# Performance work log

Hardware: AMD Instinct MI355X
Metric: run time of the kernel (lower is better)

Reference implementation:

```python
import jax, jax.numpy as jnp
import numpy as np

N_HIT = 30000   # hits per plane
N_EDGE = 90000  # Delaunay planar edges per plane (~3N)
N_SP = 30000    # spacepoints
H = 128         # hidden dim
F_IN = 4        # wire, time, integral, rms
N_CLASS = 5     # semantic classes
N_ITERS = 3     # core message-passing iterations
PLANES = ("u", "v", "y")


def setup_inputs() -> dict:
    key = jax.random.key(0)
    ks = iter(jax.random.split(key, 64))
    inp = {}
    for p in PLANES:
        inp[f"x_{p}"] = jax.random.normal(next(ks), (N_HIT, F_IN), jnp.float32)
        inp[f"edge_{p}"] = jax.random.randint(next(ks), (2, N_EDGE), 0, N_HIT)
        # row 0: hit index in plane, row 1: spacepoint index
        inp[f"nexus_{p}"] = jax.random.randint(next(ks), (2, N_SP), 0, N_HIT)
    def lin(k, i, o):
        return (jax.random.normal(k, (i, o), jnp.float32) / np.sqrt(i)).astype(jnp.float32)
    inp["W_enc"] = lin(next(ks), F_IN, H); inp["b_enc"] = jnp.zeros((H,), jnp.float32)
    inp["W_msg1"] = lin(next(ks), 2 * H, H); inp["b_msg1"] = jnp.zeros((H,), jnp.float32)
    inp["W_msg2"] = lin(next(ks), H, H); inp["b_msg2"] = jnp.zeros((H,), jnp.float32)
    inp["W_upd"] = lin(next(ks), 2 * H, H); inp["b_upd"] = jnp.zeros((H,), jnp.float32)
    inp["W_sp"] = lin(next(ks), H, H); inp["b_sp"] = jnp.zeros((H,), jnp.float32)
    inp["W_nx"] = lin(next(ks), 2 * H, H); inp["b_nx"] = jnp.zeros((H,), jnp.float32)
    inp["W_sem"] = lin(next(ks), H, N_CLASS); inp["b_sem"] = jnp.zeros((N_CLASS,), jnp.float32)
    return inp


def _segment_mean(data, ids, num):
    s = jax.ops.segment_sum(data, ids, num_segments=num)
    c = jax.ops.segment_sum(jnp.ones((ids.shape[0],), data.dtype), ids, num_segments=num)
    return s / jnp.maximum(c, 1.0)[:, None]


def _core(hs, edges, nexus, W_msg1, b_msg1, W_msg2, b_msg2, W_upd, b_upd,
          W_sp, b_sp, W_nx, b_nx):
    # --- planar convolution per plane (gather-transform-scatter) ---
    new_hs = []
    for h, e in zip(hs, edges):
        src, dst = e[0], e[1]
        m = jnp.concatenate([h[dst], h[src]], axis=-1)          # [E, 2H]
        m = jax.nn.relu(m @ W_msg1 + b_msg1) @ W_msg2 + b_msg2  # [E, H]
        agg = _segment_mean(m, dst, h.shape[0])                 # [N, H]
        upd = jax.nn.relu(jnp.concatenate([h, agg], -1) @ W_upd + b_upd)
        new_hs.append(h + upd)
    hs = new_hs
    # --- nexus convolution: planes -> spacepoints -> planes ---
    sp = jnp.zeros((N_SP, hs[0].shape[1]), hs[0].dtype)
    for h, nx in zip(hs, nexus):
        sp = sp + _segment_mean(h[nx[0]], nx[1], N_SP)
    sp = jax.nn.relu(sp @ W_sp + b_sp)                          # [N_SP, H]
    out_hs = []
    for h, nx in zip(hs, nexus):
        back = _segment_mean(sp[nx[1]], nx[0], h.shape[0])      # [N, H]
        upd = jax.nn.relu(jnp.concatenate([h, back], -1) @ W_nx + b_nx)
        out_hs.append(h + upd)
    return out_hs


def reference(x_u, x_v, x_y, edge_u, edge_v, edge_y, nexus_u, nexus_v, nexus_y,
              W_enc, b_enc, W_msg1, b_msg1, W_msg2, b_msg2, W_upd, b_upd,
              W_sp, b_sp, W_nx, b_nx, W_sem, b_sem):
    edges = (edge_u, edge_v, edge_y)
    nexus = (nexus_u, nexus_v, nexus_y)
    # encoder
    hs = [jax.nn.relu(x @ W_enc + b_enc) for x in (x_u, x_v, x_y)]
    # core message-passing iterations (planar + nexus)
    for _ in range(N_ITERS):
        hs = _core(hs, edges, nexus, W_msg1, b_msg1, W_msg2, b_msg2,
                   W_upd, b_upd, W_sp, b_sp, W_nx, b_nx)
    # semantic decoder per plane
    return tuple(h @ W_sem + b_sem for h in hs)
```

## Files before the change

kernel.cpp:

```cpp
#include <hip/hip_runtime.h>
#include <hip/hip_fp16.h>

#define N_HITS 30000
#define N_EDGES 90000
#define N_SPS 30000
#define HD 128
#define NCLS 5

#define PADM 136

typedef __attribute__((ext_vector_type(8))) _Float16 f16x8;
typedef __attribute__((ext_vector_type(4))) float floatx4;

__device__ __forceinline__ float2 h2f2(uint u) {
    union { uint u; __half2 h; } x; x.u = u;
    return __half22float2(x.h);
}
__device__ __forceinline__ uint f2h2(float a, float b) {
    union { uint u; __half2 h; } x;
    x.h = __halves2half2(__float2half(a), __float2half(b));
    return x.u;
}

__global__ void hist_all_kernel(const int* __restrict__ eu, const int* __restrict__ ev,
                                const int* __restrict__ ey, const int* __restrict__ nu,
                                const int* __restrict__ nv, const int* __restrict__ ny,
                                int* __restrict__ cnt) {
    int gid = blockIdx.x * blockDim.x + threadIdx.x;
    if (gid >= 450000) return;
    int p = gid / 150000;
    int r = gid - p * 150000;
    const int* e = (p == 0) ? eu : (p == 1) ? ev : ey;
    const int* nx = (p == 0) ? nu : (p == 1) ? nv : ny;
    if (r < N_EDGES) {
        atomicAdd(&cnt[p * 30000 + e[N_EDGES + r]], 1);
    } else if (r < N_EDGES + N_SPS) {
        int i = r - N_EDGES;
        atomicAdd(&cnt[(3 + p) * 30000 + nx[N_SPS + i]], 1);
    } else {
        int i = r - N_EDGES - N_SPS;
        atomicAdd(&cnt[(6 + p) * 30000 + nx[i]], 1);
    }
}

__launch_bounds__(1024)
__global__ void scan_kernel(const int* __restrict__ cnt, int* __restrict__ off,
                            int* __restrict__ cursor) {
    int seg = blockIdx.x;
    const int* c = cnt + seg * 30000;
    int* o = off + seg * 30001;
    int* cur = cursor + seg * 30000;
    int t = threadIdx.x;
    int base = t * 30;
    int lc[30];
    int sum = 0;
#pragma unroll
    for (int k = 0; k < 30; ++k) {
        int i = base + k;
        lc[k] = (i < 30000) ? c[i] : 0;
        sum += lc[k];
    }
    __shared__ int part[1024];
    part[t] = sum;
    __syncthreads();
    for (int d = 1; d < 1024; d <<= 1) {
        int x = (t >= d) ? part[t - d] : 0;
        __syncthreads();
        part[t] += x;
        __syncthreads();
    }
    int run = part[t] - sum;
#pragma unroll
    for (int k = 0; k < 30; ++k) {
        int i = base + k;
        if (i < 30000) { o[i] = run; cur[i] = run; run += lc[k]; }
    }
    if (t == 1023) o[30000] = part[1023];
}

__global__ void fill_kernel(const int* __restrict__ eu, const int* __restrict__ ev,
                            const int* __restrict__ ey, const int* __restrict__ nu,
                            const int* __restrict__ nv, const int* __restrict__ ny,
                            int* __restrict__ cursor, int* __restrict__ csr_e,
                            int* __restrict__ csr_s, int* __restrict__ csr_h) {
    int gid = blockIdx.x * blockDim.x + threadIdx.x;
    if (gid >= 450000) return;
    int p = gid / 150000;
    int r = gid - p * 150000;
    const int* e = (p == 0) ? eu : (p == 1) ? ev : ey;
    const int* nx = (p == 0) ? nu : (p == 1) ? nv : ny;
    if (r < N_EDGES) {
        int d = e[N_EDGES + r];
        int pos = atomicAdd(&cursor[p * 30000 + d], 1);
        csr_e[p * N_EDGES + pos] = e[r];
    } else if (r < N_EDGES + N_SPS) {
        int i = r - N_EDGES;
        int spid = nx[N_SPS + i];
        int pos = atomicAdd(&cursor[(3 + p) * 30000 + spid], 1);
        csr_s[p * N_SPS + pos] = nx[i];
    } else {
        int i = r - N_EDGES - N_SPS;
        int hit = nx[i];
        int pos = atomicAdd(&cursor[(6 + p) * 30000 + hit], 1);
        csr_h[p * N_SPS + pos] = nx[N_SPS + i];
    }
}

__device__ __forceinline__ void pack4(const float* __restrict__ W, _Float16* __restrict__ P,
                                      int idx, int koff) {
    int j = idx & 7, lane = (idx >> 3) & 63, ks = (idx >> 9) & 3, n = (idx >> 11) & 7;
    int k = ks * 32 + (lane >> 4) * 8 + j, col = n * 16 + (lane & 15);
    P[idx] = (_Float16)W[(k + koff) * 128 + col];
}
__device__ __forceinline__ void pack8(const float* __restrict__ W, _Float16* __restrict__ P, int idx) {
    int j = idx & 7, lane = (idx >> 3) & 63, ks = (idx >> 9) & 7, n = (idx >> 12) & 7;
    int k = ks * 32 + (lane >> 4) * 8 + j, col = n * 16 + (lane & 15);
    P[idx] = (_Float16)W[k * 128 + col];
}

__global__ void wprep_kernel(const float* __restrict__ W1, const float* __restrict__ W2,
                             const float* __restrict__ Wu, const float* __restrict__ Wn,
                             const float* __restrict__ Wsp, _Float16* __restrict__ packs) {
    int gid = blockIdx.x * blockDim.x + threadIdx.x;
    if (gid < 16384) { pack4(W1, packs, gid, 0); return; }
    gid -= 16384;
    if (gid < 16384) { pack4(W1, packs + 16384, gid, 128); return; }
    gid -= 16384;
    if (gid < 16384) { pack4(W2, packs + 32768, gid, 0); return; }
    gid -= 16384;
    if (gid < 32768) { pack8(Wu, packs + 49152, gid); return; }
    gid -= 32768;
    if (gid < 32768) { pack8(Wn, packs + 81920, gid); return; }
    gid -= 32768;
    if (gid < 16384) { pack4(Wsp, packs + 114688, gid, 0); }
}

__launch_bounds__(256, 4)
__global__ void enc_y_kernel(const float* __restrict__ xu, const float* __restrict__ xv,
                             const float* __restrict__ xy, const float* __restrict__ We,
                             const float* __restrict__ be, const _Float16* __restrict__ W1dP,
                             const _Float16* __restrict__ W1sP, _Float16* __restrict__ h,
                             _Float16* __restrict__ y_d, _Float16* __restrict__ y_s) {
    __shared__ _Float16 sA[128 * PADM];
    __shared__ _Float16 sO[128 * PADM];
    int t = threadIdx.x;
    int n0b = blockIdx.x * 128;
    const int M = 3 * N_HITS;
    for (int i = t; i < 2048; i += 256) {
        int row = i >> 4, c = i & 15;
        int n = n0b + row; if (n >= M) n = M - 1;
        int p = n / N_HITS;
        int nn = n - p * N_HITS;
        const float* x = (p == 0) ? xu : (p == 1) ? xv : xy;
        float4 xv4 = *(const float4*)(x + nn * 4);
        union { _Float16 o8[8]; uint4 u; } outv;
#pragma unroll
        for (int j = 0; j < 8; ++j) {
            int col = c * 8 + j;
            float acc = be[col];
            acc = fmaf(xv4.x, We[0 * HD + col], acc);
            acc = fmaf(xv4.y, We[1 * HD + col], acc);
            acc = fmaf(xv4.z, We[2 * HD + col], acc);
            acc = fmaf(xv4.w, We[3 * HD + col], acc);
            outv.o8[j] = (_Float16)fmaxf(acc, 0.f);
        }
        *(uint4*)&sA[row * PADM + c * 8] = outv.u;
        if (n0b + row < M) ((uint4*)(h + (size_t)n * HD))[c] = outv.u;
    }
    __syncthreads();

    int lane = t & 63, wave = t >> 6;
    int lcol = lane & 15, quad = lane >> 4;
    int nt0 = wave * 2;
    bool odd = (lcol & 1) != 0;

    for (int half = 0; half < 2; ++half) {
        const f16x8* wp = (const f16x8*)(half == 0 ? W1dP : W1sP);
        _Float16* out = half == 0 ? y_d : y_s;
        f16x8 B[2][4];
#pragma unroll
        for (int nt = 0; nt < 2; ++nt)
#pragma unroll
            for (int ks = 0; ks < 4; ++ks)
                B[nt][ks] = wp[((nt0 + nt) * 4 + ks) * 64 + lane];
        floatx4 acc[8][2];
#pragma unroll
        for (int mt = 0; mt < 8; ++mt) { acc[mt][0] = (floatx4){0,0,0,0}; acc[mt][1] = (floatx4){0,0,0,0}; }
#pragma unroll
        for (int mt = 0; mt < 8; ++mt)
#pragma unroll
            for (int ks = 0; ks < 4; ++ks) {
                f16x8 a = *(const f16x8*)&sA[(mt * 16 + lcol) * PADM + ks * 32 + quad * 8];
                acc[mt][0] = __builtin_amdgcn_mfma_f32_16x16x32_f16(a, B[0][ks], acc[mt][0], 0, 0, 0);
                acc[mt][1] = __builtin_amdgcn_mfma_f32_16x16x32_f16(a, B[1][ks], acc[mt][1], 0, 0, 0);
            }
#pragma unroll
        for (int mt = 0; mt < 8; ++mt)
#pragma unroll
            for (int r = 0; r < 4; ++r) {
                float v0 = acc[mt][0][r], v1 = acc[mt][1][r];
                float p0 = __shfl_xor(v0, 1), p1 = __shfl_xor(v1, 1);
                float av = odd ? p1 : v0, bv = odd ? v1 : p0;
                int col = nt0 * 16 + (odd ? 15 + lcol : lcol);
                *(uint*)&sO[(mt * 16 + quad * 4 + r) * PADM + col] = f2h2(av, bv);
            }
        __syncthreads();
        for (int i = t; i < 2048; i += 256) {
            int row = i >> 4, c = i & 15;
            int n = n0b + row;
            if (n < M) ((uint4*)(out + (size_t)n * HD))[c] = *(uint4*)&sO[row * PADM + c * 8];
        }
        __syncthreads();
    }
}

#define ECAP 640
__launch_bounds__(256, 5)
__global__ void update_planar_kernel(_Float16* __restrict__ h, const _Float16* __restrict__ y_d,
                                     const _Float16* __restrict__ y_s,
                                     const int* __restrict__ off, const int* __restrict__ csr_e,
                                     const float* __restrict__ b1,
                                     const _Float16* __restrict__ W2P, const float* __restrict__ b2,
                                     const _Float16* __restrict__ WuP, const float* __restrict__ bu) {
    int p = blockIdx.y;
    _Float16* hp = h + (size_t)p * N_HITS * HD;
    const _Float16* ydp = y_d + (size_t)p * N_HITS * HD;
    const _Float16* ysp = y_s + (size_t)p * N_HITS * HD;
    const int* o = off + p * 30001;
    const int* csr = csr_e + p * N_EDGES;

    __shared__ _Float16 sA[64 * PADM];
    __shared__ int sOff[65];
    __shared__ int sIdx[ECAP];
    int t = threadIdx.x;
    int n0b = blockIdx.x * 64;
    int lane = t & 63, wave = t >> 6;
    int lcol = lane & 15, quad = lane >> 4;
    int nt0 = wave * 2;
    bool odd = (lcol & 1) != 0;

    if (t < 65) {
        int idx = n0b + t; if (idx > N_HITS) idx = N_HITS;
        sOff[t] = o[idx];
    }
    for (int i = t; i < 1024; i += 256) {
        int row = i >> 4, c = i & 15;
        int n = n0b + row; if (n >= N_HITS) n = N_HITS - 1;
        f16x8 yv = *(const f16x8*)&ydp[(size_t)n * HD + c * 8];
        float4 b1a = *(const float4*)(b1 + c * 8);
        float4 b1b = *(const float4*)(b1 + c * 8 + 4);
        float bb[8] = {b1a.x, b1a.y, b1a.z, b1a.w, b1b.x, b1b.y, b1b.z, b1b.w};
        f16x8 ov;
#pragma unroll
        for (int j = 0; j < 8; ++j) ov[j] = (_Float16)((float)yv[j] + bb[j]);
        *(f16x8*)&sA[row * PADM + c * 8] = ov;
    }
    __syncthreads();
    int base = sOff[0];
    int total = sOff[64] - base;
    bool useL = (total <= ECAP);
    if (useL) for (int i = t; i < total; i += 256) sIdx[i] = csr[base + i];
    __syncthreads();

    for (int i = t; i < 1024; i += 256) {
        int row = i >> 4, c = i & 15;
        int d = n0b + row;
        int beg = 0, end = 0;
        if (d < N_HITS) { beg = sOff[row]; end = sOff[row + 1]; }
        f16x8 ydv = *(const f16x8*)&sA[row * PADM + c * 8];
        f16x8 a0 = (f16x8)(_Float16)0, a1 = (f16x8)(_Float16)0;
        int k = beg;
        for (; k + 2 <= end; k += 2) {
            int s0 = useL ? sIdx[k - base] : csr[k];
            int s1 = useL ? sIdx[k + 1 - base] : csr[k + 1];
            f16x8 y0 = *(const f16x8*)&ysp[(size_t)s0 * HD + c * 8];
            f16x8 y1 = *(const f16x8*)&ysp[(size_t)s1 * HD + c * 8];
            a0 += __builtin_elementwise_max(y0 + ydv, (f16x8)(_Float16)0);
            a1 += __builtin_elementwise_max(y1 + ydv, (f16x8)(_Float16)0);
        }
        if (k < end) {
            int s0 = useL ? sIdx[k - base] : csr[k];
            f16x8 y0 = *(const f16x8*)&ysp[(size_t)s0 * HD + c * 8];
            a0 += __builtin_elementwise_max(y0 + ydv, (f16x8)(_Float16)0);
        }
        f16x8 accv = a0 + a1;
        _Float16 iv = (_Float16)((end > beg) ? 1.f / (float)(end - beg) : 0.f);
        accv *= iv;
        *(f16x8*)&sA[row * PADM + c * 8] = accv;
    }
    __syncthreads();
    floatx4 acc[4][2];
    {
        const f16x8* w2p = (const f16x8*)W2P;
        f16x8 B[2][4];
#pragma unroll
        for (int nt = 0; nt < 2; ++nt)
#pragma unroll
            for (int ks = 0; ks < 4; ++ks)
                B[nt][ks] = w2p[((nt0 + nt) * 4 + ks) * 64 + lane];
#pragma unroll
        for (int nt = 0; nt < 2; ++nt) {
            float bv = b2[(nt0 + nt) * 16 + lcol];
#pragma unroll
            for (int mt = 0; mt < 4; ++mt) acc[mt][nt] = (floatx4){bv, bv, bv, bv};
        }
#pragma unroll
        for (int mt = 0; mt < 4; ++mt)
#pragma unroll
            for (int ks = 0; ks < 4; ++ks) {
                f16x8 a = *(const f16x8*)&sA[(mt * 16 + lcol) * PADM + ks * 32 + quad * 8];
                acc[mt][0] = __builtin_amdgcn_mfma_f32_16x16x32_f16(a, B[0][ks], acc[mt][0], 0, 0, 0);
                acc[mt][1] = __builtin_amdgcn_mfma_f32_16x16x32_f16(a, B[1][ks], acc[mt][1], 0, 0, 0);
            }
    }
    __syncthreads();
#pragma unroll
    for (int mt = 0; mt < 4; ++mt)
#pragma unroll
        for (int r = 0; r < 4; ++r) {
            float v0 = acc[mt][0][r], v1 = acc[mt][1][r];
            float p0 = __shfl_xor(v0, 1), p1 = __shfl_xor(v1, 1);
            float av = odd ? p1 : v0, bv = odd ? v1 : p0;
            int col = nt0 * 16 + (odd ? 15 + lcol : lcol);
            *(uint*)&sA[(mt * 16 + quad * 4 + r) * PADM + col] = f2h2(av, bv);
        }
    __syncthreads();
    {
        const f16x8* wu = (const f16x8*)WuP;
        f16x8 B[2][4];
#pragma unroll
        for (int nt = 0; nt < 2; ++nt)
#pragma unroll
            for (int ks = 0; ks < 4; ++ks)
                B[nt][ks] = wu[((nt0 + nt) * 8 + 4 + ks) * 64 + lane];
        floatx4 tmp[4][2];
#pragma unroll
        for (int nt = 0; nt < 2; ++nt) {
            float bv = bu[(nt0 + nt) * 16 + lcol];
#pragma unroll
            for (int mt = 0; mt < 4; ++mt) tmp[mt][nt] = (floatx4){bv, bv, bv, bv};
        }
#pragma unroll
        for (int mt = 0; mt < 4; ++mt)
#pragma unroll
            for (int ks = 0; ks < 4; ++ks) {
                f16x8 a = *(const f16x8*)&sA[(mt * 16 + lcol) * PADM + ks * 32 + quad * 8];
                tmp[mt][0] = __builtin_amdgcn_mfma_f32_16x16x32_f16(a, B[0][ks], tmp[mt][0], 0, 0, 0);
                tmp[mt][1] = __builtin_amdgcn_mfma_f32_16x16x32_f16(a, B[1][ks], tmp[mt][1], 0, 0, 0);
            }
#pragma unroll
        for (int mt = 0; mt < 4; ++mt) { acc[mt][0] = tmp[mt][0]; acc[mt][1] = tmp[mt][1]; }
    }
    __syncthreads();
    for (int i = t; i < 1024; i += 256) {
        int row = i >> 4, c = i & 15;
        int n = n0b + row; if (n >= N_HITS) n = N_HITS - 1;
        *(uint4*)&sA[row * PADM + c * 8] = ((const uint4*)(hp + (size_t)n * HD))[c];
    }
    __syncthreads();
    {
        const f16x8* wu = (const f16x8*)WuP;
        f16x8 B[2][4];
#pragma unroll
        for (int nt = 0; nt < 2; ++nt)
#pragma unroll
            for (int ks = 0; ks < 4; ++ks)
                B[nt][ks] = wu[((nt0 + nt) * 8 + ks) * 64 + lane];
#pragma unroll
        for (int mt = 0; mt < 4; ++mt)
#pragma unroll
            for (int ks = 0; ks < 4; ++ks) {
                f16x8 a = *(const f16x8*)&sA[(mt * 16 + lcol) * PADM + ks * 32 + quad * 8];
                acc[mt][0] = __builtin_amdgcn_mfma_f32_16x16x32_f16(a, B[0][ks], acc[mt][0], 0, 0, 0);
                acc[mt][1] = __builtin_amdgcn_mfma_f32_16x16x32_f16(a, B[1][ks], acc[mt][1], 0, 0, 0);
            }
    }
    __syncthreads();
#pragma unroll
    for (int mt = 0; mt < 4; ++mt)
#pragma unroll
        for (int r = 0; r < 4; ++r) {
            float v0 = fmaxf(acc[mt][0][r], 0.f), v1 = fmaxf(acc[mt][1][r], 0.f);
            float p0 = __shfl_xor(v0, 1), p1 = __shfl_xor(v1, 1);
            float av = odd ? p1 : v0, bv = odd ? v1 : p0;
            int col = nt0 * 16 + (odd ? 15 + lcol : lcol);
            uint* sp2 = (uint*)&sA[(mt * 16 + quad * 4 + r) * PADM + col];
            float2 ho = h2f2(*sp2);
            *sp2 = f2h2(ho.x + av, ho.y + bv);
        }
    __syncthreads();
    for (int i = t; i < 1024; i += 256) {
        int row = i >> 4, c = i & 15;
        int n = n0b + row;
        if (n < N_HITS) ((uint4*)(hp + (size_t)n * HD))[c] = *(uint4*)&sA[row * PADM + c * 8];
    }
}

#define SCAP 576
__launch_bounds__(256, 6)
__global__ void sp_fused_kernel(const _Float16* __restrict__ h, const int* __restrict__ off,
                                const int* __restrict__ csr_s, const _Float16* __restrict__ WspP,
                                const float* __restrict__ b, _Float16* __restrict__ spf) {
    __shared__ _Float16 sA[64 * PADM];
    __shared__ int sOff[3][65];
    __shared__ int sIdx[SCAP];
    int t = threadIdx.x;
    int n0b = blockIdx.x * 64;
    int lane = t & 63, wave = t >> 6;
    int lcol = lane & 15, quad = lane >> 4;
    int nt0 = wave * 2;
    bool odd = (lcol & 1) != 0;

    if (t < 195) {
        int p = t / 65, i = t - p * 65;
        int idx = n0b + i; if (idx > N_SPS) idx = N_SPS;
        sOff[p][i] = off[(3 + p) * 30001 + idx];
    }
    __syncthreads();
    int base0 = sOff[0][0], len0 = sOff[0][64] - base0;
    int base1 = sOff[1][0], len1 = sOff[1][64] - base1;
    int base2 = sOff[2][0], len2 = sOff[2][64] - base2;
    int ofs1 = len0, ofs2 = len0 + len1;
    bool useL = (ofs2 + len2 <= SCAP);
    if (useL) {
        for (int i = t; i < len0; i += 256) sIdx[i] = csr_s[base0 + i];
        for (int i = t; i < len1; i += 256) sIdx[ofs1 + i] = csr_s[N_SPS + base1 + i];
        for (int i = t; i < len2; i += 256) sIdx[ofs2 + i] = csr_s[2 * N_SPS + base2 + i];
    }
    __syncthreads();

    for (int i = t; i < 1024; i += 256) {
        int row = i >> 4, c = i & 15;
        int s = n0b + row;
        f16x8 tv = (f16x8)(_Float16)0;
        if (s < N_SPS) {
#pragma unroll
            for (int p = 0; p < 3; ++p) {
                int beg = sOff[p][row], end = sOff[p][row + 1];
                int bb = (p == 0) ? base0 : (p == 1) ? base1 : base2;
                int oo = (p == 0) ? 0 : (p == 1) ? ofs1 : ofs2;
                const int* csr = csr_s + p * N_SPS;
                const _Float16* hb = h + (size_t)p * N_HITS * HD;
                f16x8 s0v = (f16x8)(_Float16)0, s1v = (f16x8)(_Float16)0;
                int k = beg;
                for (; k + 2 <= end; k += 2) {
                    int h0 = useL ? sIdx[oo + (k - bb)] : csr[k];
                    int h1 = useL ? sIdx[oo + (k + 1 - bb)] : csr[k + 1];
                    f16x8 v0 = *(const f16x8*)&hb[(size_t)h0 * HD + c * 8];
                    f16x8 v1 = *(const f16x8*)&hb[(size_t)h1 * HD + c * 8];
                    s0v += v0; s1v += v1;
                }
                if (k < end) {
                    int h0 = useL ? sIdx[oo + (k - bb)] : csr[k];
                    s0v += *(const f16x8*)&hb[(size_t)h0 * HD + c * 8];
                }
                f16x8 sv = s0v + s1v;
                _Float16 iv = (_Float16)((end > beg) ? 1.f / (float)(end - beg) : 0.f);
                tv += sv * iv;
            }
        }
        *(f16x8*)&sA[row * PADM + c * 8] = tv;
    }
    __syncthreads();

    const f16x8* wp = (const f16x8*)WspP;
    f16x8 B[2][4];
#pragma unroll
    for (int nt = 0; nt < 2; ++nt)
#pragma unroll
        for (int ks = 0; ks < 4; ++ks)
            B[nt][ks] = wp[((nt0 + nt) * 4 + ks) * 64 + lane];

    floatx4 acc[4][2];
#pragma unroll
    for (int nt = 0; nt < 2; ++nt) {
        float bv = b[(nt0 + nt) * 16 + lcol];
#pragma unroll
        for (int mt = 0; mt < 4; ++mt) acc[mt][nt] = (floatx4){bv, bv, bv, bv};
    }
#pragma unroll
    for (int mt = 0; mt < 4; ++mt)
#pragma unroll
        for (int ks = 0; ks < 4; ++ks) {
            f16x8 a = *(const f16x8*)&sA[(mt * 16 + lcol) * PADM + ks * 32 + quad * 8];
            acc[mt][0] = __builtin_amdgcn_mfma_f32_16x16x32_f16(a, B[0][ks], acc[mt][0], 0, 0, 0);
            acc[mt][1] = __builtin_amdgcn_mfma_f32_16x16x32_f16(a, B[1][ks], acc[mt][1], 0, 0, 0);
        }
    __syncthreads();
#pragma unroll
    for (int mt = 0; mt < 4; ++mt)
#pragma unroll
        for (int r = 0; r < 4; ++r) {
            float v0 = fmaxf(acc[mt][0][r], 0.f), v1 = fmaxf(acc[mt][1][r], 0.f);
            float p0 = __shfl_xor(v0, 1), p1 = __shfl_xor(v1, 1);
            float av = odd ? p1 : v0, bv = odd ? v1 : p0;
            int col = nt0 * 16 + (odd ? 15 + lcol : lcol);
            *(uint*)&sA[(mt * 16 + quad * 4 + r) * PADM + col] = f2h2(av, bv);
        }
    __syncthreads();
    for (int i = t; i < 1024; i += 256) {
        int row = i >> 4, c = i & 15;
        int n = n0b + row;
        if (n < N_SPS) ((uint4*)(spf + (size_t)n * HD))[c] = *(uint4*)&sA[row * PADM + c * 8];
    }
}

#define HCAP 320
__launch_bounds__(256, 4)
__global__ void update_y_kernel(_Float16* __restrict__ h, const _Float16* __restrict__ sp,
                                const int* __restrict__ off, const int* __restrict__ csr_h,
                                const _Float16* __restrict__ WP, const float* __restrict__ b,
                                const _Float16* __restrict__ W1dP, const _Float16* __restrict__ W1sP,
                                _Float16* __restrict__ y_d, _Float16* __restrict__ y_s) {
    int p = blockIdx.y;
    _Float16* hp = h + (size_t)p * N_HITS * HD;
    _Float16* ydp = y_d + (size_t)p * N_HITS * HD;
    _Float16* ysp = y_s + (size_t)p * N_HITS * HD;
    const int* o = off + (6 + p) * 30001;
    const int* csr = csr_h + p * N_SPS;

    __shared__ _Float16 sH[64 * PADM];
    __shared__ _Float16 sA[64 * PADM];
    __shared__ int sOff[65];
    __shared__ int sIdx[HCAP];
    int t = threadIdx.x;
    int n0b = blockIdx.x * 64;
    int lane = t & 63, wave = t >> 6;
    int lcol = lane & 15, quad = lane >> 4;
    int nt0 = wave * 2;
    bool odd = (lcol & 1) != 0;

    if (t < 65) {
        int idx = n0b + t; if (idx > N_HITS) idx = N_HITS;
        sOff[t] = o[idx];
    }
    for (int i = t; i < 1024; i += 256) {
        int row = i >> 4, c = i & 15;
        int n = n0b + row; if (n >= N_HITS) n = N_HITS - 1;
        *(uint4*)&sH[row * PADM + c * 8] = ((const uint4*)(hp + (size_t)n * HD))[c];
    }
    __syncthreads();
    int base = sOff[0];
    int total = sOff[64] - base;
    bool useL = (total <= HCAP);
    if (useL) for (int i = t; i < total; i += 256) sIdx[i] = csr[base + i];
    __syncthreads();

    for (int i = t; i < 1024; i += 256) {
        int row = i >> 4, c = i & 15;
        int hit = n0b + row;
        int beg = 0, end = 0;
        if (hit < N_HITS) { beg = sOff[row]; end = sOff[row + 1]; }
        f16x8 a0 = (f16x8)(_Float16)0, a1 = (f16x8)(_Float16)0;
        int k = beg;
        for (; k + 2 <= end; k += 2) {
            int s0 = useL ? sIdx[k - base] : csr[k];
            int s1 = useL ? sIdx[k + 1 - base] : csr[k + 1];
            f16x8 v0 = *(const f16x8*)&sp[(size_t)s0 * HD + c * 8];
            f16x8 v1 = *(const f16x8*)&sp[(size_t)s1 * HD + c * 8];
            a0 += v0; a1 += v1;
        }
        if (k < end) {
            int s0 = useL ? sIdx[k - base] : csr[k];
            a0 += *(const f16x8*)&sp[(size_t)s0 * HD + c * 8];
        }
        f16x8 av8 = a0 + a1;
        _Float16 iv = (_Float16)((end > beg) ? 1.f / (float)(end - beg) : 0.f);
        av8 *= iv;
        *(f16x8*)&sA[row * PADM + c * 8] = av8;
    }
    __syncthreads();
    floatx4 acc[4][2];
    {
        const f16x8* wp = (const f16x8*)WP;
        f16x8 BH[2][4], BA[2][4];
#pragma unroll
        for (int nt = 0; nt < 2; ++nt)
#pragma unroll
            for (int ks = 0; ks < 4; ++ks) {
                BH[nt][ks] = wp[((nt0 + nt) * 8 + ks) * 64 + lane];
                BA[nt][ks] = wp[((nt0 + nt) * 8 + 4 + ks) * 64 + lane];
            }
#pragma unroll
        for (int nt = 0; nt < 2; ++nt) {
            float bv = b[(nt0 + nt) * 16 + lcol];
#pragma unroll
            for (int mt = 0; mt < 4; ++mt) acc[mt][nt] = (floatx4){bv, bv, bv, bv};
        }
#pragma unroll
        for (int mt = 0; mt < 4; ++mt)
#pragma unroll
            for (int ks = 0; ks < 4; ++ks) {
                f16x8 ah = *(const f16x8*)&sH[(mt * 16 + lcol) * PADM + ks * 32 + quad * 8];
                f16x8 aa = *(const f16x8*)&sA[(mt * 16 + lcol) * PADM + ks * 32 + quad * 8];
                acc[mt][0] = __builtin_amdgcn_mfma_f32_16x16x32_f16(ah, BH[0][ks], acc[mt][0], 0, 0, 0);
                acc[mt][1] = __builtin_amdgcn_mfma_f32_16x16x32_f16(ah, BH[1][ks], acc[mt][1], 0, 0, 0);
                acc[mt][0] = __builtin_amdgcn_mfma_f32_16x16x32_f16(aa, BA[0][ks], acc[mt][0], 0, 0, 0);
                acc[mt][1] = __builtin_amdgcn_mfma_f32_16x16x32_f16(aa, BA[1][ks], acc[mt][1], 0, 0, 0);
            }
    }
    __syncthreads();
#pragma unroll
    for (int mt = 0; mt < 4; ++mt)
#pragma unroll
        for (int r = 0; r < 4; ++r) {
            float v0 = fmaxf(acc[mt][0][r], 0.f), v1 = fmaxf(acc[mt][1][r], 0.f);
            float p0 = __shfl_xor(v0, 1), p1 = __shfl_xor(v1, 1);
            float av = odd ? p1 : v0, bv = odd ? v1 : p0;
            int col = nt0 * 16 + (odd ? 15 + lcol : lcol);
            uint* sp2 = (uint*)&sH[(mt * 16 + quad * 4 + r) * PADM + col];
            float2 ho = h2f2(*sp2);
            *sp2 = f2h2(ho.x + av, ho.y + bv);
        }
    __syncthreads();
    for (int i = t; i < 1024; i += 256) {
        int row = i >> 4, c = i & 15;
        int n = n0b + row;
        if (n < N_HITS) ((uint4*)(hp + (size_t)n * HD))[c] = *(uint4*)&sH[row * PADM + c * 8];
    }
    for (int half = 0; half < 2; ++half) {
        const f16x8* wyp = (const f16x8*)(half == 0 ? W1sP : W1dP);
        _Float16* out = half == 0 ? ysp : ydp;
        f16x8 B[2][4];
#pragma unroll
        for (int nt = 0; nt < 2; ++nt)
#pragma unroll
            for (int ks = 0; ks < 4; ++ks)
                B[nt][ks] = wyp[((nt0 + nt) * 4 + ks) * 64 + lane];
        floatx4 yacc[4][2];
#pragma unroll
        for (int mt = 0; mt < 4; ++mt) { yacc[mt][0] = (floatx4){0,0,0,0}; yacc[mt][1] = (floatx4){0,0,0,0}; }
#pragma unroll
        for (int mt = 0; mt < 4; ++mt)
#pragma unroll
            for (int ks = 0; ks < 4; ++ks) {
                f16x8 a = *(const f16x8*)&sH[(mt * 16 + lcol) * PADM + ks * 32 + quad * 8];
                yacc[mt][0] = __builtin_amdgcn_mfma_f32_16x16x32_f16(a, B[0][ks], yacc[mt][0], 0, 0, 0);
                yacc[mt][1] = __builtin_amdgcn_mfma_f32_16x16x32_f16(a, B[1][ks], yacc[mt][1], 0, 0, 0);
            }
        __syncthreads();
#pragma unroll
        for (int mt = 0; mt < 4; ++mt)
#pragma unroll
            for (int r = 0; r < 4; ++r) {
                float v0 = yacc[mt][0][r], v1 = yacc[mt][1][r];
                float p0 = __shfl_xor(v0, 1), p1 = __shfl_xor(v1, 1);
                float av = odd ? p1 : v0, bv = odd ? v1 : p0;
                int col = nt0 * 16 + (odd ? 15 + lcol : lcol);
                *(uint*)&sA[(mt * 16 + quad * 4 + r) * PADM + col] = f2h2(av, bv);
            }
        __syncthreads();
        for (int i = t; i < 1024; i += 256) {
            int row = i >> 4, c = i & 15;
            int n = n0b + row;
            if (n < N_HITS) ((uint4*)(out + (size_t)n * HD))[c] = *(uint4*)&sA[row * PADM + c * 8];
        }
    }
}

__global__ void dec_kernel(const _Float16* __restrict__ h, const float* __restrict__ W,
                           const float* __restrict__ b, float* __restrict__ out) {
    __shared__ float sW[640];
    __shared__ float sB[8];
    int t = threadIdx.x;
    for (int i = t; i < 640; i += 256) sW[i] = W[i];
    if (t < 5) sB[t] = b[t];
    __syncthreads();
    int n = blockIdx.x * 256 + t;
    if (n >= 3 * N_HITS) return;
    const uint4* hr = (const uint4*)(h + (size_t)n * HD);
    float a0 = sB[0], a1 = sB[1], a2 = sB[2], a3 = sB[3], a4 = sB[4];
#pragma unroll 4
    for (int q = 0; q < 16; ++q) {
        union { uint4 u; _Float16 hh[8]; } v; v.u = hr[q];
        const float* w = &sW[q * 40];
#pragma unroll
        for (int j = 0; j < 8; ++j) {
            float x = (float)v.hh[j];
            a0 = fmaf(x, w[j * 5 + 0], a0);
            a1 = fmaf(x, w[j * 5 + 1], a1);
            a2 = fmaf(x, w[j * 5 + 2], a2);
            a3 = fmaf(x, w[j * 5 + 3], a3);
            a4 = fmaf(x, w[j * 5 + 4], a4);
        }
    }
    float* oo = out + (size_t)n * NCLS;
    oo[0] = a0; oo[1] = a1; oo[2] = a2; oo[3] = a3; oo[4] = a4;
}

extern "C" void kernel_launch(void* const* d_in, const int* in_sizes, int n_in,
                              void* d_out, int out_size, void* d_ws, size_t ws_size,
                              hipStream_t stream) {
    const float* xu = (const float*)d_in[0];
    const int* eu = (const int*)d_in[1];
    const int* nu = (const int*)d_in[2];
    const float* xv = (const float*)d_in[3];
    const int* ev = (const int*)d_in[4];
    const int* nv = (const int*)d_in[5];
    const float* xy = (const float*)d_in[6];
    const int* ey = (const int*)d_in[7];
    const int* ny = (const int*)d_in[8];
    const float* W_enc = (const float*)d_in[9];
    const float* b_enc = (const float*)d_in[10];
    const float* W1 = (const float*)d_in[11];
    const float* b1 = (const float*)d_in[12];
    const float* W2 = (const float*)d_in[13];
    const float* b2 = (const float*)d_in[14];
    const float* W_upd = (const float*)d_in[15];
    const float* b_upd = (const float*)d_in[16];
    const float* W_sp = (const float*)d_in[17];
    const float* b_sp = (const float*)d_in[18];
    const float* W_nx = (const float*)d_in[19];
    const float* b_nx = (const float*)d_in[20];
    const float* W_sem = (const float*)d_in[21];
    const float* b_sem = (const float*)d_in[22];

    const size_t HN = (size_t)3 * N_HITS * HD;
    _Float16* h = (_Float16*)d_ws;
    _Float16* y_s = h + HN;
    _Float16* y_d = y_s + HN;
    _Float16* sp = y_d + HN;
    int* cnt = (int*)(sp + (size_t)N_SPS * HD);
    int* off = cnt + 270000;
    int* cursor = off + 270009;
    int* csr_e = cursor + 270000;
    int* csr_s = csr_e + 270000;
    int* csr_h = csr_s + 90000;
    _Float16* packs = (_Float16*)(csr_h + 90000);
    _Float16* W1dP = packs;
    _Float16* W1sP = packs + 16384;
    _Float16* W2P = packs + 32768;
    _Float16* WuP = packs + 49152;
    _Float16* WnP = packs + 81920;
    _Float16* WspP = packs + 114688;

    wprep_kernel<<<512, 256, 0, stream>>>(W1, W2, W_upd, W_nx, W_sp, packs);
    (void)hipMemsetAsync(cnt, 0, 270000 * sizeof(int), stream);
    hist_all_kernel<<<(450000 + 255) / 256, 256, 0, stream>>>(eu, ev, ey, nu, nv, ny, cnt);
    scan_kernel<<<9, 1024, 0, stream>>>(cnt, off, cursor);
    fill_kernel<<<(450000 + 255) / 256, 256, 0, stream>>>(eu, ev, ey, nu, nv, ny,
                                                          cursor, csr_e, csr_s, csr_h);

    enc_y_kernel<<<(3 * N_HITS + 127) / 128, 256, 0, stream>>>(xu, xv, xy, W_enc, b_enc,
                                                               W1dP, W1sP, h, y_d, y_s);

    for (int it = 0; it < 3; ++it) {
        update_planar_kernel<<<dim3((N_HITS + 63) / 64, 3), 256, 0, stream>>>(
            h, y_d, y_s, off, csr_e, b1, W2P, b2, WuP, b_upd);
        sp_fused_kernel<<<(N_SPS + 63) / 64, 256, 0, stream>>>(h, off, csr_s, WspP, b_sp, sp);
        update_y_kernel<<<dim3((N_HITS + 63) / 64, 3), 256, 0, stream>>>(
            h, sp, off, csr_h, WnP, b_nx, W1dP, W1sP, y_d, y_s);
    }

    dec_kernel<<<(3 * N_HITS + 255) / 256, 256, 0, stream>>>(h, W_sem, b_sem, (float*)d_out);
}
```

Before: 493.8 us.

## Fuse semantic decoder into last update kernel and peel gather loops

Removes the separate decoder kernel: on the final iteration, update_y computes the 5-class projection directly from the updated hidden tile held in shared memory, reduces the partial sums with lane shuffles, and skips the now-unneeded y_d/y_s projection GEMMs. It also adds a peeled first batch of up to four (planar) or two (nexus) neighbor loads in the gather loops so that more independent memory loads are in flight. The peeled prologue adds branching and register pressure, and the decoder reads W_sem from global memory per thread instead of from shared memory.

```diff
diff --git a/kernel.cpp b/kernel.cpp
--- a/kernel.cpp
+++ b/kernel.cpp
@@ -269,21 +269,38 @@
         if (d < N_HITS) { beg = sOff[row]; end = sOff[row + 1]; }
         f16x8 ydv = *(const f16x8*)&sA[row * PADM + c * 8];
         f16x8 a0 = (f16x8)(_Float16)0, a1 = (f16x8)(_Float16)0;
+        f16x8 a2 = (f16x8)(_Float16)0, a3 = (f16x8)(_Float16)0;
         int k = beg;
+        int rem = end - beg;
+        if (rem > 0) {
+            int s0 = useL ? sIdx[k - base] : csr[k];
+            int s1 = (rem > 1) ? (useL ? sIdx[k + 1 - base] : csr[k + 1]) : s0;
+            int s2 = (rem > 2) ? (useL ? sIdx[k + 2 - base] : csr[k + 2]) : s0;
+            int s3 = (rem > 3) ? (useL ? sIdx[k + 3 - base] : csr[k + 3]) : s0;
+            f16x8 v0 = *(const f16x8*)&ysp[(size_t)s0 * HD + c * 8];
+            f16x8 v1 = *(const f16x8*)&ysp[(size_t)s1 * HD + c * 8];
+            f16x8 v2 = *(const f16x8*)&ysp[(size_t)s2 * HD + c * 8];
+            f16x8 v3 = *(const f16x8*)&ysp[(size_t)s3 * HD + c * 8];
+            a0 += __builtin_elementwise_max(v0 + ydv, (f16x8)(_Float16)0);
+            if (rem > 1) a1 += __builtin_elementwise_max(v1 + ydv, (f16x8)(_Float16)0);
+            if (rem > 2) a2 += __builtin_elementwise_max(v2 + ydv, (f16x8)(_Float16)0);
+            if (rem > 3) a3 += __builtin_elementwise_max(v3 + ydv, (f16x8)(_Float16)0);
+            k += (rem < 4) ? rem : 4;
+        }
         for (; k + 2 <= end; k += 2) {
             int s0 = useL ? sIdx[k - base] : csr[k];
             int s1 = useL ? sIdx[k + 1 - base] : csr[k + 1];
-            f16x8 y0 = *(const f16x8*)&ysp[(size_t)s0 * HD + c * 8];
-            f16x8 y1 = *(const f16x8*)&ysp[(size_t)s1 * HD + c * 8];
-            a0 += __builtin_elementwise_max(y0 + ydv, (f16x8)(_Float16)0);
-            a1 += __builtin_elementwise_max(y1 + ydv, (f16x8)(_Float16)0);
+            f16x8 v0 = *(const f16x8*)&ysp[(size_t)s0 * HD + c * 8];
+            f16x8 v1 = *(const f16x8*)&ysp[(size_t)s1 * HD + c * 8];
+            a0 += __builtin_elementwise_max(v0 + ydv, (f16x8)(_Float16)0);
+            a1 += __builtin_elementwise_max(v1 + ydv, (f16x8)(_Float16)0);
         }
         if (k < end) {
             int s0 = useL ? sIdx[k - base] : csr[k];
-            f16x8 y0 = *(const f16x8*)&ysp[(size_t)s0 * HD + c * 8];
-            a0 += __builtin_elementwise_max(y0 + ydv, (f16x8)(_Float16)0);
-        }
-        f16x8 accv = a0 + a1;
+            f16x8 v0 = *(const f16x8*)&ysp[(size_t)s0 * HD + c * 8];
+            a0 += __builtin_elementwise_max(v0 + ydv, (f16x8)(_Float16)0);
+        }
+        f16x8 accv = (a0 + a1) + (a2 + a3);
         _Float16 iv = (_Float16)((end > beg) ? 1.f / (float)(end - beg) : 0.f);
         accv *= iv;
         *(f16x8*)&sA[row * PADM + c * 8] = accv;
@@ -443,6 +460,16 @@
                 const _Float16* hb = h + (size_t)p * N_HITS * HD;
                 f16x8 s0v = (f16x8)(_Float16)0, s1v = (f16x8)(_Float16)0;
                 int k = beg;
+                int rem = end - beg;
+                if (rem > 0) {
+                    int h0 = useL ? sIdx[oo + (k - bb)] : csr[k];
+                    int h1 = (rem > 1) ? (useL ? sIdx[oo + (k + 1 - bb)] : csr[k + 1]) : h0;
+                    f16x8 v0 = *(const f16x8*)&hb[(size_t)h0 * HD + c * 8];
+                    f16x8 v1 = *(const f16x8*)&hb[(size_t)h1 * HD + c * 8];
+                    s0v += v0;
+                    if (rem > 1) s1v += v1;
+                    k += (rem < 2) ? rem : 2;
+                }
                 for (; k + 2 <= end; k += 2) {
                     int h0 = useL ? sIdx[oo + (k - bb)] : csr[k];
                     int h1 = useL ? sIdx[oo + (k + 1 - bb)] : csr[k + 1];
@@ -511,7 +538,9 @@
                                 const int* __restrict__ off, const int* __restrict__ csr_h,
                                 const _Float16* __restrict__ WP, const float* __restrict__ b,
                                 const _Float16* __restrict__ W1dP, const _Float16* __restrict__ W1sP,
-                                _Float16* __restrict__ y_d, _Float16* __restrict__ y_s) {
+                                _Float16* __restrict__ y_d, _Float16* __restrict__ y_s,
+                                const float* __restrict__ Wsem, const float* __restrict__ bsem,
+                                float* __restrict__ out, int last) {
     int p = blockIdx.y;
     _Float16* hp = h + (size_t)p * N_HITS * HD;
     _Float16* ydp = y_d + (size_t)p * N_HITS * HD;
@@ -553,6 +582,16 @@
         if (hit < N_HITS) { beg = sOff[row]; end = sOff[row + 1]; }
         f16x8 a0 = (f16x8)(_Float16)0, a1 = (f16x8)(_Float16)0;
         int k = beg;
+        int rem = end - beg;
+        if (rem > 0) {
+            int s0 = useL ? sIdx[k - base] : csr[k];
+            int s1 = (rem > 1) ? (useL ? sIdx[k + 1 - base] : csr[k + 1]) : s0;
+            f16x8 v0 = *(const f16x8*)&sp[(size_t)s0 * HD + c * 8];
+            f16x8 v1 = *(const f16x8*)&sp[(size_t)s1 * HD + c * 8];
+            a0 += v0;
+            if (rem > 1) a1 += v1;
+            k += (rem < 2) ? rem : 2;
+        }
         for (; k + 2 <= end; k += 2) {
             int s0 = useL ? sIdx[k - base] : csr[k];
             int s1 = useL ? sIdx[k + 1 - base] : csr[k + 1];
@@ -618,9 +657,40 @@
         int n = n0b + row;
         if (n < N_HITS) ((uint4*)(hp + (size_t)n * HD))[c] = *(uint4*)&sH[row * PADM + c * 8];
     }
+    if (last) {
+        int row = t >> 2, part = t & 3;
+        int n = n0b + row;
+        float a0 = 0.f, a1 = 0.f, a2 = 0.f, a3 = 0.f, a4 = 0.f;
+        const _Float16* hr = &sH[row * PADM + part * 32];
+#pragma unroll
+        for (int q = 0; q < 4; ++q) {
+            f16x8 v = *(const f16x8*)(hr + q * 8);
+#pragma unroll
+            for (int j = 0; j < 8; ++j) {
+                float x = (float)v[j];
+                const float* w = Wsem + (part * 32 + q * 8 + j) * NCLS;
+                a0 = fmaf(x, w[0], a0);
+                a1 = fmaf(x, w[1], a1);
+                a2 = fmaf(x, w[2], a2);
+                a3 = fmaf(x, w[3], a3);
+                a4 = fmaf(x, w[4], a4);
+            }
+        }
+        a0 += __shfl_xor(a0, 1); a0 += __shfl_xor(a0, 2);
+        a1 += __shfl_xor(a1, 1); a1 += __shfl_xor(a1, 2);
+        a2 += __shfl_xor(a2, 1); a2 += __shfl_xor(a2, 2);
+        a3 += __shfl_xor(a3, 1); a3 += __shfl_xor(a3, 2);
+        a4 += __shfl_xor(a4, 1); a4 += __shfl_xor(a4, 2);
+        if (part == 0 && n < N_HITS) {
+            float* oo = out + ((size_t)p * N_HITS + n) * NCLS;
+            oo[0] = a0 + bsem[0]; oo[1] = a1 + bsem[1]; oo[2] = a2 + bsem[2];
+            oo[3] = a3 + bsem[3]; oo[4] = a4 + bsem[4];
+        }
+        return;
+    }
     for (int half = 0; half < 2; ++half) {
         const f16x8* wyp = (const f16x8*)(half == 0 ? W1sP : W1dP);
-        _Float16* out = half == 0 ? ysp : ydp;
+        _Float16* outy = half == 0 ? ysp : ydp;
         f16x8 B[2][4];
 #pragma unroll
         for (int nt = 0; nt < 2; ++nt)
@@ -653,39 +723,9 @@
         for (int i = t; i < 1024; i += 256) {
             int row = i >> 4, c = i & 15;
             int n = n0b + row;
-            if (n < N_HITS) ((uint4*)(out + (size_t)n * HD))[c] = *(uint4*)&sA[row * PADM + c * 8];
-        }
-    }
-}
-
-__global__ void dec_kernel(const _Float16* __restrict__ h, const float* __restrict__ W,
-                           const float* __restrict__ b, float* __restrict__ out) {
-    __shared__ float sW[640];
-    __shared__ float sB[8];
-    int t = threadIdx.x;
-    for (int i = t; i < 640; i += 256) sW[i] = W[i];
-    if (t < 5) sB[t] = b[t];
-    __syncthreads();
-    int n = blockIdx.x * 256 + t;
-    if (n >= 3 * N_HITS) return;
-    const uint4* hr = (const uint4*)(h + (size_t)n * HD);
-    float a0 = sB[0], a1 = sB[1], a2 = sB[2], a3 = sB[3], a4 = sB[4];
-#pragma unroll 4
-    for (int q = 0; q < 16; ++q) {
-        union { uint4 u; _Float16 hh[8]; } v; v.u = hr[q];
-        const float* w = &sW[q * 40];
-#pragma unroll
-        for (int j = 0; j < 8; ++j) {
-            float x = (float)v.hh[j];
-            a0 = fmaf(x, w[j * 5 + 0], a0);
-            a1 = fmaf(x, w[j * 5 + 1], a1);
-            a2 = fmaf(x, w[j * 5 + 2], a2);
-            a3 = fmaf(x, w[j * 5 + 3], a3);
-            a4 = fmaf(x, w[j * 5 + 4], a4);
-        }
-    }
-    float* oo = out + (size_t)n * NCLS;
-    oo[0] = a0; oo[1] = a1; oo[2] = a2; oo[3] = a3; oo[4] = a4;
+            if (n < N_HITS) ((uint4*)(outy + (size_t)n * HD))[c] = *(uint4*)&sA[row * PADM + c * 8];
+        }
+    }
 }
 
 extern "C" void kernel_launch(void* const* d_in, const int* in_sizes, int n_in,
@@ -749,8 +789,7 @@
             h, y_d, y_s, off, csr_e, b1, W2P, b2, WuP, b_upd);
         sp_fused_kernel<<<(N_SPS + 63) / 64, 256, 0, stream>>>(h, off, csr_s, WspP, b_sp, sp);
         update_y_kernel<<<dim3((N_HITS + 63) / 64, 3), 256, 0, stream>>>(
-            h, sp, off, csr_h, WnP, b_nx, W1dP, W1sP, y_d, y_s);
-    }
-
-    dec_kernel<<<(3 * N_HITS + 255) / 256, 256, 0, stream>>>(h, W_sem, b_sem, (float*)d_out);
-}
+            h, sp, off, csr_h, WnP, b_nx, W1dP, W1sP, y_d, y_s,
+            W_sem, b_sem, (float*)d_out, it == 2 ? 1 : 0);
+    }
+}
```

Result: no change. 492.2 us (median of 2 runs) (-0.3%).
